# Optimization experiments

Hardware: AMD Instinct MI355X
Metric: run time of the kernel (lower is better)

Reference implementation:

```python
import jax, jax.numpy as jnp
import numpy as np

B, S, D_IN, D_OUT = 4, 2048, 4096, 4096
ACT_BITS = 8
GROUP_SIZE = 64
EPS = 1e-5


def _ste(x, q):
    # straight-through estimator: forward value q, gradient of identity
    return x + jax.lax.stop_gradient(q - x)


def absmax_quantize_dequant(x, bits=ACT_BITS, group_size=GROUP_SIZE):
    # per-token, per-group absmax fake quantization along the last dim
    qmax = float(2 ** (bits - 1) - 1)  # 127 for 8 bits
    *lead, d = x.shape
    g = group_size if group_size is not None else d
    xg = x.reshape(*lead, d // g, g)
    absmax = jnp.max(jnp.abs(xg), axis=-1, keepdims=True)
    scale = qmax / jnp.clip(absmax, EPS, None)
    q = jnp.clip(jnp.round(xg * scale), -qmax, qmax) / scale
    q = q.reshape(*lead, d)
    return _ste(x, q)


def ternary_weight_quantize_absmean(w, per_row=True):
    # BitNet b1.58: scale = mean(|W|) per output row; W_t in {-s, 0, s}
    axis = (1,) if per_row else (0, 1)
    s = jnp.mean(jnp.abs(w), axis=axis, keepdims=True)
    s = jnp.clip(s, EPS, None)
    q = jnp.clip(jnp.round(w / s), -1.0, 1.0) * s
    return _ste(w, q)


def setup_inputs() -> dict:
    key = jax.random.key(0)
    k1, k2 = jax.random.split(key)
    x = jax.random.normal(k1, (B, S, D_IN), dtype=jnp.float32)
    # kaiming-uniform-ish init scale
    bound = float(np.sqrt(1.0 / D_IN))
    weight = jax.random.uniform(k2, (D_OUT, D_IN), dtype=jnp.float32,
                                minval=-bound, maxval=bound)
    return {"x": x, "weight": weight}


def reference(x, weight):
    x_q = absmax_quantize_dequant(x)                      # [B,S,D_in]
    w_t = ternary_weight_quantize_absmean(weight)         # [D_out,D_in]
    return jnp.einsum("bsi,oi->bso", x_q, w_t)            # [B,S,D_out]
```

## Files before the change

kernel.cpp:

```cpp
#include <hip/hip_runtime.h>
#include <hip/hip_bf16.h>
#include <stdint.h>

constexpr int M = 4 * 2048;
constexpr int K = 4096;
constexpr int N = 4096;
constexpr float EPSf = 1e-5f;
constexpr float QMAX = 127.0f;

typedef __attribute__((ext_vector_type(8))) short bf16x8;
typedef __attribute__((ext_vector_type(4))) float f32x4;

__device__ __forceinline__ unsigned short f2bf(float f) {
  union { float f; uint32_t u; } c; c.f = f;
  uint32_t u = c.u;
  return (unsigned short)((u + 0x7fffu + ((u >> 16) & 1u)) >> 16);
}

__device__ __forceinline__ void async_copy16(const void* g, const void* l) {
  __builtin_amdgcn_global_load_lds(
      (const __attribute__((address_space(1))) unsigned int*)g,
      (__attribute__((address_space(3))) unsigned int*)l, 16, 0, 0);
}

__global__ void __launch_bounds__(256) quant_x_kernel(const float* __restrict__ x,
                                                      unsigned short* __restrict__ xq) {
  const int t = blockIdx.x * 256 + threadIdx.x;
  const float4 v = ((const float4*)x)[t];
  float m = fmaxf(fmaxf(fabsf(v.x), fabsf(v.y)), fmaxf(fabsf(v.z), fabsf(v.w)));
  #pragma unroll
  for (int d = 1; d < 16; d <<= 1) m = fmaxf(m, __shfl_xor(m, d));
  m = fmaxf(m, EPSf);
  const float scale = QMAX / m;

  float q0 = fminf(fmaxf(rintf(v.x * scale), -QMAX), QMAX);
  float q1 = fminf(fmaxf(rintf(v.y * scale), -QMAX), QMAX);
  float q2 = fminf(fmaxf(rintf(v.z * scale), -QMAX), QMAX);
  float q3 = fminf(fmaxf(rintf(v.w * scale), -QMAX), QMAX);
  ushort4 o;
  o.x = f2bf(q0 / scale);
  o.y = f2bf(q1 / scale);
  o.z = f2bf(q2 / scale);
  o.w = f2bf(q3 / scale);
  ((ushort4*)xq)[t] = o;
}

__global__ void __launch_bounds__(256) quant_w_kernel(const float* __restrict__ w,
                                                      unsigned short* __restrict__ wt,
                                                      float* __restrict__ wscale) {
  const int row = blockIdx.x;
  const int tid = threadIdx.x;
  const float* wr = w + (long)row * K;
  float4 v[4];
  float s = 0.f;
  #pragma unroll
  for (int p = 0; p < 4; p++) {
    v[p] = ((const float4*)wr)[tid + p * 256];
    s += fabsf(v[p].x) + fabsf(v[p].y) + fabsf(v[p].z) + fabsf(v[p].w);
  }
  #pragma unroll
  for (int d = 1; d < 64; d <<= 1) s += __shfl_xor(s, d);
  __shared__ float red[4];
  if ((tid & 63) == 0) red[tid >> 6] = s;
  __syncthreads();
  const float tot = red[0] + red[1] + red[2] + red[3];
  const float sc = fmaxf(tot / (float)K, EPSf);
  if (tid == 0) wscale[row] = sc;
  unsigned short* wrow = wt + (long)row * K;
  #pragma unroll
  for (int p = 0; p < 4; p++) {
    ushort4 o;
    o.x = f2bf(fminf(fmaxf(rintf(v[p].x / sc), -1.f), 1.f));
    o.y = f2bf(fminf(fmaxf(rintf(v[p].y / sc), -1.f), 1.f));
    o.z = f2bf(fminf(fmaxf(rintf(v[p].z / sc), -1.f), 1.f));
    o.w = f2bf(fminf(fmaxf(rintf(v[p].w / sc), -1.f), 1.f));
    ((ushort4*)wrow)[tid + p * 256] = o;
  }
}

__global__ void __launch_bounds__(256) gemm_bt_kernel(const short* __restrict__ A,
                                                      const short* __restrict__ Bt,
                                                      const float* __restrict__ wscale,
                                                      float* __restrict__ C) {
  __shared__ short sA[128 * 32];
  __shared__ short sB[128 * 32];

  const int n0 = blockIdx.x * 128;
  const int m0 = blockIdx.y * 128;
  const int tid  = (int)threadIdx.x;
  const int lane = tid & 63;
  const int wv   = tid >> 6;
  const int wm = wv & 1, wn = wv >> 1;
  const int quad = lane >> 4, r16 = lane & 15;

  const int srow = tid >> 2;
  const int scol = (tid & 3) * 8;

  f32x4 acc[4][4];
  #pragma unroll
  for (int i = 0; i < 4; i++)
    #pragma unroll
    for (int j = 0; j < 4; j++) acc[i][j] = (f32x4){0.f, 0.f, 0.f, 0.f};

  const short* Ab = A  + (long)m0 * K;
  const short* Bb = Bt + (long)n0 * K;

  for (int k0 = 0; k0 < K; k0 += 32) {
    async_copy16(Ab + (long)srow * K        + k0 + scol, sA + tid * 8);
    async_copy16(Ab + (long)(srow + 64) * K + k0 + scol, sA + 2048 + tid * 8);
    async_copy16(Bb + (long)srow * K        + k0 + scol, sB + tid * 8);
    async_copy16(Bb + (long)(srow + 64) * K + k0 + scol, sB + 2048 + tid * 8);
    asm volatile("s_waitcnt vmcnt(0)" ::: "memory");
    __syncthreads();

    bf16x8 a[4], b[4];
    #pragma unroll
    for (int i = 0; i < 4; i++)
      a[i] = *(const bf16x8*)(sA + (wm * 64 + i * 16 + r16) * 32 + quad * 8);
    #pragma unroll
    for (int j = 0; j < 4; j++)
      b[j] = *(const bf16x8*)(sB + (wn * 64 + j * 16 + r16) * 32 + quad * 8);
    #pragma unroll
    for (int i = 0; i < 4; i++)
      #pragma unroll
      for (int j = 0; j < 4; j++)
        acc[i][j] = __builtin_amdgcn_mfma_f32_16x16x32_bf16(a[i], b[j], acc[i][j], 0, 0, 0);
    __syncthreads();
  }

  #pragma unroll
  for (int j = 0; j < 4; j++) {
    const int col = n0 + wn * 64 + j * 16 + r16;
    const float sc = wscale[col];
    #pragma unroll
    for (int i = 0; i < 4; i++) {
      const int rbase = m0 + wm * 64 + i * 16 + quad * 4;
      #pragma unroll
      for (int r = 0; r < 4; r++)
        C[(long)(rbase + r) * N + col] = acc[i][j][r] * sc;
    }
  }
}

extern "C" void kernel_launch(void* const* d_in, const int* in_sizes, int n_in,
                              void* d_out, int out_size, void* d_ws, size_t ws_size,
                              hipStream_t stream) {
  const float* x   = (const float*)d_in[0];
  const float* wgt = (const float*)d_in[1];
  float* out = (float*)d_out;

  unsigned short* Aq = (unsigned short*)d_ws;
  unsigned short* Tq = Aq + (size_t)M * K;
  float* wscale = (float*)(Tq + (size_t)N * K);

  quant_x_kernel<<<(M * K / 4) / 256, 256, 0, stream>>>(x, Aq);
  quant_w_kernel<<<N, 256, 0, stream>>>(wgt, Tq, wscale);

  dim3 grid(N / 128, M / 128);
  gemm_bt_kernel<<<grid, 256, 0, stream>>>((const short*)Aq, (const short*)Tq,
                                           wscale, out);
}
```

Baseline: 557.2 us.

## Double-buffer GEMM LDS tiles, switch to 32x32 MFMA, fuse quant kernels

The GEMM now double-buffers A and B tiles in LDS so the async global-to-LDS copy of the next K-slice is issued before the current slice's MFMAs. It also uses 32x32x16 bf16 MFMA with a fragment-friendly LDS layout instead of 16x16x32. The two quantization kernels are merged into a single launch that branches on block index. Correctness relies on the barrier implicitly waiting for the outstanding global_load_lds copies, since the explicit vmcnt wait was removed.

```diff
diff --git a/kernel.cpp b/kernel.cpp
--- a/kernel.cpp
+++ b/kernel.cpp
@@ -9,7 +9,7 @@
 constexpr float QMAX = 127.0f;
 
 typedef __attribute__((ext_vector_type(8))) short bf16x8;
-typedef __attribute__((ext_vector_type(4))) float f32x4;
+typedef __attribute__((ext_vector_type(16))) float f32x16;
 
 __device__ __forceinline__ unsigned short f2bf(float f) {
   union { float f; uint32_t u; } c; c.f = f;
@@ -23,67 +23,77 @@
       (__attribute__((address_space(3))) unsigned int*)l, 16, 0, 0);
 }
 
-__global__ void __launch_bounds__(256) quant_x_kernel(const float* __restrict__ x,
-                                                      unsigned short* __restrict__ xq) {
-  const int t = blockIdx.x * 256 + threadIdx.x;
-  const float4 v = ((const float4*)x)[t];
-  float m = fmaxf(fmaxf(fabsf(v.x), fabsf(v.y)), fmaxf(fabsf(v.z), fabsf(v.w)));
-  #pragma unroll
-  for (int d = 1; d < 16; d <<= 1) m = fmaxf(m, __shfl_xor(m, d));
-  m = fmaxf(m, EPSf);
-  const float scale = QMAX / m;
-
-  float q0 = fminf(fmaxf(rintf(v.x * scale), -QMAX), QMAX);
-  float q1 = fminf(fmaxf(rintf(v.y * scale), -QMAX), QMAX);
-  float q2 = fminf(fmaxf(rintf(v.z * scale), -QMAX), QMAX);
-  float q3 = fminf(fmaxf(rintf(v.w * scale), -QMAX), QMAX);
-  ushort4 o;
-  o.x = f2bf(q0 / scale);
-  o.y = f2bf(q1 / scale);
-  o.z = f2bf(q2 / scale);
-  o.w = f2bf(q3 / scale);
-  ((ushort4*)xq)[t] = o;
-}
-
-__global__ void __launch_bounds__(256) quant_w_kernel(const float* __restrict__ w,
-                                                      unsigned short* __restrict__ wt,
-                                                      float* __restrict__ wscale) {
-  const int row = blockIdx.x;
+constexpr int XBLOCKS = (M * K / 4) / 256;
+
+__global__ void __launch_bounds__(256) quant_fused_kernel(
+    const float* __restrict__ x, const float* __restrict__ w,
+    unsigned short* __restrict__ xq, unsigned short* __restrict__ wt,
+    float* __restrict__ wscale) {
   const int tid = threadIdx.x;
-  const float* wr = w + (long)row * K;
-  float4 v[4];
-  float s = 0.f;
-  #pragma unroll
-  for (int p = 0; p < 4; p++) {
-    v[p] = ((const float4*)wr)[tid + p * 256];
-    s += fabsf(v[p].x) + fabsf(v[p].y) + fabsf(v[p].z) + fabsf(v[p].w);
+  if (blockIdx.x < XBLOCKS) {
+    const int t = blockIdx.x * 256 + tid;
+    const float4 v = ((const float4*)x)[t];
+    float m = fmaxf(fmaxf(fabsf(v.x), fabsf(v.y)), fmaxf(fabsf(v.z), fabsf(v.w)));
+    #pragma unroll
+    for (int d = 1; d < 16; d <<= 1) m = fmaxf(m, __shfl_xor(m, d));
+    m = fmaxf(m, EPSf);
+    const float scale = QMAX / m;
+    float q0 = fminf(fmaxf(rintf(v.x * scale), -QMAX), QMAX);
+    float q1 = fminf(fmaxf(rintf(v.y * scale), -QMAX), QMAX);
+    float q2 = fminf(fmaxf(rintf(v.z * scale), -QMAX), QMAX);
+    float q3 = fminf(fmaxf(rintf(v.w * scale), -QMAX), QMAX);
+    ushort4 o;
+    o.x = f2bf(q0 / scale);
+    o.y = f2bf(q1 / scale);
+    o.z = f2bf(q2 / scale);
+    o.w = f2bf(q3 / scale);
+    ((ushort4*)xq)[t] = o;
+  } else {
+    const int row = blockIdx.x - XBLOCKS;
+    const float* wr = w + (long)row * K;
+    float4 v[4];
+    float s = 0.f;
+    #pragma unroll
+    for (int p = 0; p < 4; p++) {
+      v[p] = ((const float4*)wr)[tid + p * 256];
+      s += fabsf(v[p].x) + fabsf(v[p].y) + fabsf(v[p].z) + fabsf(v[p].w);
+    }
+    #pragma unroll
+    for (int d = 1; d < 64; d <<= 1) s += __shfl_xor(s, d);
+    __shared__ float red[4];
+    if ((tid & 63) == 0) red[tid >> 6] = s;
+    __syncthreads();
+    const float tot = red[0] + red[1] + red[2] + red[3];
+    const float sc = fmaxf(tot / (float)K, EPSf);
+    if (tid == 0) wscale[row] = sc;
+    unsigned short* wrow = wt + (long)row * K;
+    #pragma unroll
+    for (int p = 0; p < 4; p++) {
+      ushort4 o;
+      o.x = f2bf(fminf(fmaxf(rintf(v[p].x / sc), -1.f), 1.f));
+      o.y = f2bf(fminf(fmaxf(rintf(v[p].y / sc), -1.f), 1.f));
+      o.z = f2bf(fminf(fmaxf(rintf(v[p].z / sc), -1.f), 1.f));
+      o.w = f2bf(fminf(fmaxf(rintf(v[p].w / sc), -1.f), 1.f));
+      ((ushort4*)wrow)[tid + p * 256] = o;
+    }
   }
-  #pragma unroll
-  for (int d = 1; d < 64; d <<= 1) s += __shfl_xor(s, d);
-  __shared__ float red[4];
-  if ((tid & 63) == 0) red[tid >> 6] = s;
-  __syncthreads();
-  const float tot = red[0] + red[1] + red[2] + red[3];
-  const float sc = fmaxf(tot / (float)K, EPSf);
-  if (tid == 0) wscale[row] = sc;
-  unsigned short* wrow = wt + (long)row * K;
-  #pragma unroll
-  for (int p = 0; p < 4; p++) {
-    ushort4 o;
-    o.x = f2bf(fminf(fmaxf(rintf(v[p].x / sc), -1.f), 1.f));
-    o.y = f2bf(fminf(fmaxf(rintf(v[p].y / sc), -1.f), 1.f));
-    o.z = f2bf(fminf(fmaxf(rintf(v[p].z / sc), -1.f), 1.f));
-    o.w = f2bf(fminf(fmaxf(rintf(v[p].w / sc), -1.f), 1.f));
-    ((ushort4*)wrow)[tid + p * 256] = o;
-  }
+}
+
+__device__ __forceinline__ void stage_tile(const short* __restrict__ gsrc,
+                                           short* __restrict__ lbase,
+                                           int tid, int k0) {
+  const int row = (tid & 31) + ((tid >> 7) << 5);
+  const int col = ((tid >> 5) & 3) * 8;
+  async_copy16(gsrc + (long)row * K + k0 + col, lbase + tid * 8);
+  async_copy16(gsrc + (long)(row + 64) * K + k0 + col, lbase + 2048 + tid * 8);
 }
 
 __global__ void __launch_bounds__(256) gemm_bt_kernel(const short* __restrict__ A,
                                                       const short* __restrict__ Bt,
                                                       const float* __restrict__ wscale,
                                                       float* __restrict__ C) {
-  __shared__ short sA[128 * 32];
-  __shared__ short sB[128 * 32];
+  __shared__ short sA[2][128 * 32];
+  __shared__ short sB[2][128 * 32];
 
   const int n0 = blockIdx.x * 128;
   const int m0 = blockIdx.y * 128;
@@ -91,53 +101,94 @@
   const int lane = tid & 63;
   const int wv   = tid >> 6;
   const int wm = wv & 1, wn = wv >> 1;
-  const int quad = lane >> 4, r16 = lane & 15;
-
-  const int srow = tid >> 2;
-  const int scol = (tid & 3) * 8;
-
-  f32x4 acc[4][4];
+  const int ln = lane & 31;
+  const int kh = lane >> 5;
+
+  f32x16 acc[2][2];
   #pragma unroll
-  for (int i = 0; i < 4; i++)
-    #pragma unroll
-    for (int j = 0; j < 4; j++) acc[i][j] = (f32x4){0.f, 0.f, 0.f, 0.f};
+  for (int i = 0; i < 2; i++)
+    #pragma unroll
+    for (int j = 0; j < 2; j++)
+      #pragma unroll
+      for (int r = 0; r < 16; r++) acc[i][j][r] = 0.f;
 
   const short* Ab = A  + (long)m0 * K;
   const short* Bb = Bt + (long)n0 * K;
 
-  for (int k0 = 0; k0 < K; k0 += 32) {
-    async_copy16(Ab + (long)srow * K        + k0 + scol, sA + tid * 8);
-    async_copy16(Ab + (long)(srow + 64) * K + k0 + scol, sA + 2048 + tid * 8);
-    async_copy16(Bb + (long)srow * K        + k0 + scol, sB + tid * 8);
-    async_copy16(Bb + (long)(srow + 64) * K + k0 + scol, sB + 2048 + tid * 8);
-    asm volatile("s_waitcnt vmcnt(0)" ::: "memory");
-    __syncthreads();
-
-    bf16x8 a[4], b[4];
-    #pragma unroll
-    for (int i = 0; i < 4; i++)
-      a[i] = *(const bf16x8*)(sA + (wm * 64 + i * 16 + r16) * 32 + quad * 8);
-    #pragma unroll
-    for (int j = 0; j < 4; j++)
-      b[j] = *(const bf16x8*)(sB + (wn * 64 + j * 16 + r16) * 32 + quad * 8);
-    #pragma unroll
-    for (int i = 0; i < 4; i++)
+  const int fA0 = (((wm * 2 + 0) * 4 + kh) * 32 + ln) * 8;
+  const int fA1 = (((wm * 2 + 1) * 4 + kh) * 32 + ln) * 8;
+  const int fB0 = (((wn * 2 + 0) * 4 + kh) * 32 + ln) * 8;
+  const int fB1 = (((wn * 2 + 1) * 4 + kh) * 32 + ln) * 8;
+  constexpr int SOFF = 2 * 32 * 8;
+
+  stage_tile(Ab, sA[0], tid, 0);
+  stage_tile(Bb, sB[0], tid, 0);
+  __syncthreads();
+
+  #pragma unroll 1
+  for (int k0 = 0; k0 < K; k0 += 64) {
+    {
+      stage_tile(Ab, sA[1], tid, k0 + 32);
+      stage_tile(Bb, sB[1], tid, k0 + 32);
+      const short* sAc = sA[0];
+      const short* sBc = sB[0];
+      bf16x8 a0s0 = *(const bf16x8*)(sAc + fA0);
+      bf16x8 a1s0 = *(const bf16x8*)(sAc + fA1);
+      bf16x8 b0s0 = *(const bf16x8*)(sBc + fB0);
+      bf16x8 b1s0 = *(const bf16x8*)(sBc + fB1);
+      bf16x8 a0s1 = *(const bf16x8*)(sAc + fA0 + SOFF);
+      bf16x8 a1s1 = *(const bf16x8*)(sAc + fA1 + SOFF);
+      bf16x8 b0s1 = *(const bf16x8*)(sBc + fB0 + SOFF);
+      bf16x8 b1s1 = *(const bf16x8*)(sBc + fB1 + SOFF);
+      acc[0][0] = __builtin_amdgcn_mfma_f32_32x32x16_bf16(a0s0, b0s0, acc[0][0], 0, 0, 0);
+      acc[0][1] = __builtin_amdgcn_mfma_f32_32x32x16_bf16(a0s0, b1s0, acc[0][1], 0, 0, 0);
+      acc[1][0] = __builtin_amdgcn_mfma_f32_32x32x16_bf16(a1s0, b0s0, acc[1][0], 0, 0, 0);
+      acc[1][1] = __builtin_amdgcn_mfma_f32_32x32x16_bf16(a1s0, b1s0, acc[1][1], 0, 0, 0);
+      acc[0][0] = __builtin_amdgcn_mfma_f32_32x32x16_bf16(a0s1, b0s1, acc[0][0], 0, 0, 0);
+      acc[0][1] = __builtin_amdgcn_mfma_f32_32x32x16_bf16(a0s1, b1s1, acc[0][1], 0, 0, 0);
+      acc[1][0] = __builtin_amdgcn_mfma_f32_32x32x16_bf16(a1s1, b0s1, acc[1][0], 0, 0, 0);
+      acc[1][1] = __builtin_amdgcn_mfma_f32_32x32x16_bf16(a1s1, b1s1, acc[1][1], 0, 0, 0);
+      __syncthreads();
+    }
+    {
+      if (k0 + 64 < K) {
+        stage_tile(Ab, sA[0], tid, k0 + 64);
+        stage_tile(Bb, sB[0], tid, k0 + 64);
+      }
+      const short* sAc = sA[1];
+      const short* sBc = sB[1];
+      bf16x8 a0s0 = *(const bf16x8*)(sAc + fA0);
+      bf16x8 a1s0 = *(const bf16x8*)(sAc + fA1);
+      bf16x8 b0s0 = *(const bf16x8*)(sBc + fB0);
+      bf16x8 b1s0 = *(const bf16x8*)(sBc + fB1);
+      bf16x8 a0s1 = *(const bf16x8*)(sAc + fA0 + SOFF);
+      bf16x8 a1s1 = *(const bf16x8*)(sAc + fA1 + SOFF);
+      bf16x8 b0s1 = *(const bf16x8*)(sBc + fB0 + SOFF);
+      bf16x8 b1s1 = *(const bf16x8*)(sBc + fB1 + SOFF);
+      acc[0][0] = __builtin_amdgcn_mfma_f32_32x32x16_bf16(a0s0, b0s0, acc[0][0], 0, 0, 0);
+      acc[0][1] = __builtin_amdgcn_mfma_f32_32x32x16_bf16(a0s0, b1s0, acc[0][1], 0, 0, 0);
+      acc[1][0] = __builtin_amdgcn_mfma_f32_32x32x16_bf16(a1s0, b0s0, acc[1][0], 0, 0, 0);
+      acc[1][1] = __builtin_amdgcn_mfma_f32_32x32x16_bf16(a1s0, b1s0, acc[1][1], 0, 0, 0);
+      acc[0][0] = __builtin_amdgcn_mfma_f32_32x32x16_bf16(a0s1, b0s1, acc[0][0], 0, 0, 0);
+      acc[0][1] = __builtin_amdgcn_mfma_f32_32x32x16_bf16(a0s1, b1s1, acc[0][1], 0, 0, 0);
+      acc[1][0] = __builtin_amdgcn_mfma_f32_32x32x16_bf16(a1s1, b0s1, acc[1][0], 0, 0, 0);
+      acc[1][1] = __builtin_amdgcn_mfma_f32_32x32x16_bf16(a1s1, b1s1, acc[1][1], 0, 0, 0);
+      __syncthreads();
+    }
+  }
+
+  #pragma unroll
+  for (int jb = 0; jb < 2; jb++) {
+    const int col = n0 + wn * 64 + jb * 32 + ln;
+    const float sc = wscale[col];
+    #pragma unroll
+    for (int ib = 0; ib < 2; ib++) {
+      const int rbase = m0 + wm * 64 + ib * 32 + 4 * kh;
       #pragma unroll
-      for (int j = 0; j < 4; j++)
-        acc[i][j] = __builtin_amdgcn_mfma_f32_16x16x32_bf16(a[i], b[j], acc[i][j], 0, 0, 0);
-    __syncthreads();
-  }
-
-  #pragma unroll
-  for (int j = 0; j < 4; j++) {
-    const int col = n0 + wn * 64 + j * 16 + r16;
-    const float sc = wscale[col];
-    #pragma unroll
-    for (int i = 0; i < 4; i++) {
-      const int rbase = m0 + wm * 64 + i * 16 + quad * 4;
-      #pragma unroll
-      for (int r = 0; r < 4; r++)
-        C[(long)(rbase + r) * N + col] = acc[i][j][r] * sc;
+      for (int r = 0; r < 16; r++) {
+        const int row = rbase + (r & 3) + 8 * (r >> 2);
+        C[(long)row * N + col] = acc[ib][jb][r] * sc;
+      }
     }
   }
 }
@@ -153,8 +204,7 @@
   unsigned short* Tq = Aq + (size_t)M * K;
   float* wscale = (float*)(Tq + (size_t)N * K);
 
-  quant_x_kernel<<<(M * K / 4) / 256, 256, 0, stream>>>(x, Aq);
-  quant_w_kernel<<<N, 256, 0, stream>>>(wgt, Tq, wscale);
+  quant_fused_kernel<<<XBLOCKS + N, 256, 0, stream>>>(x, wgt, Aq, Tq, wscale);
 
   dim3 grid(N / 128, M / 128);
   gemm_bt_kernel<<<grid, 256, 0, stream>>>((const short*)Aq, (const short*)Tq,
```

Measured after the change: 748.7 us. 34.4% more time.
